# Kernel optimization log

Hardware: AMD Instinct MI355X
Metric: run time of the kernel (lower is better)

## Reference

```python
import jax, jax.numpy as jnp
import numpy as np

B, T, D, F, C = 16384, 256, 8, 512, 16  # batch, trees, depth, features, classes
L = 2 ** D  # leaves per tree


def setup_inputs() -> dict:
    key = jax.random.key(0)
    k1, k2, k3, k4 = jax.random.split(key, 4)
    x = jax.random.normal(k1, (B, F), dtype=jnp.float32)
    feature_weights = jax.random.normal(k2, (T, D, F), dtype=jnp.float32)
    thresholds = jax.random.normal(k3, (T, D), dtype=jnp.float32)
    responses = jax.random.normal(k4, (T, L, C), dtype=jnp.float32)
    return {"x": x, "feature_weights": feature_weights,
            "thresholds": thresholds, "responses": responses}


def reference(x, feature_weights, thresholds, responses):
    # Hard feature selection per (tree, level): argmax over features.
    fidx = jnp.argmax(feature_weights, axis=-1)            # [T, D] int
    fv = x[:, fidx]                                        # [B, T, D] gather
    bits = (fv > thresholds[None, :, :]).astype(x.dtype)   # [B, T, D]
    # decision = sum_d bit_d * 2^(D-1-d)  (matches decision*2+bit loop)
    powers = (2 ** jnp.arange(D - 1, -1, -1)).astype(x.dtype)  # [D]
    decision = jnp.sum(bits * powers, axis=-1).astype(jnp.int32)  # [B, T]
    # Gather leaf responses per (sample, tree) and average over trees.
    tree_ids = jnp.arange(T)[None, :]                      # [1, T]
    leaf_out = responses[tree_ids, decision]               # [B, T, C]
    out = jnp.mean(leaf_out, axis=1)                       # [B, C]
    return out  # dropout is identity at eval time
```

## Files before the change

kernel.cpp:

```cpp
#include <hip/hip_runtime.h>

constexpr int B = 16384;
constexpr int T = 256;
constexpr int D = 8;
constexpr int F = 512;
constexpr int C = 16;
constexpr int L = 256;

struct FP { int fidx; float thr; };

__global__ __launch_bounds__(256) void node_prep_kernel(
    const float* __restrict__ fw,
    const float* __restrict__ thr,
    FP* __restrict__ packed)
{
    const int wave = threadIdx.x >> 6;
    const int lane = threadIdx.x & 63;
    const int row  = blockIdx.x * 4 + wave;
    const float* base = fw + (size_t)row * F;

    float best = -INFINITY;
    int bidx = 0;
#pragma unroll
    for (int k = 0; k < F / 64; ++k) {
        const int idx = lane + k * 64;
        const float v = base[idx];
        if (v > best) { best = v; bidx = idx; }
    }
#pragma unroll
    for (int off = 32; off >= 1; off >>= 1) {
        const float ov = __shfl_xor(best, off);
        const int   oi = __shfl_xor(bidx, off);
        if (ov > best || (ov == best && oi < bidx)) { best = ov; bidx = oi; }
    }
    if (lane == 0) {
        FP p;
        p.fidx = bidx;
        p.thr  = thr[row];
        packed[row] = p;
    }
}

__global__ __launch_bounds__(256) void forest_kernel(
    const float* __restrict__ x,
    const FP* __restrict__ packed,
    const float* __restrict__ responses,
    float* __restrict__ out)
{
    __shared__ float xrow[4][F];
    __shared__ unsigned char sdec[4][T];

    const int b0  = blockIdx.x * 4;
    const int tid = threadIdx.x;

    {
        const float4* xs = reinterpret_cast<const float4*>(x + (size_t)b0 * F);
        float4* xl = reinterpret_cast<float4*>(&xrow[0][0]);
        xl[tid]       = xs[tid];
        xl[tid + 256] = xs[tid + 256];
    }
    __syncthreads();

    {
        const int2* p2 = reinterpret_cast<const int2*>(packed) + tid * D;
        int2 raw[D];
#pragma unroll
        for (int d = 0; d < D; ++d) raw[d] = p2[d];
        int dec0 = 0, dec1 = 0, dec2 = 0, dec3 = 0;
#pragma unroll
        for (int d = 0; d < D; ++d) {
            const int   f  = raw[d].x;
            const float th = __int_as_float(raw[d].y);
            const int   p  = 128 >> d;
            dec0 |= (xrow[0][f] > th) ? p : 0;
            dec1 |= (xrow[1][f] > th) ? p : 0;
            dec2 |= (xrow[2][f] > th) ? p : 0;
            dec3 |= (xrow[3][f] > th) ? p : 0;
        }
        sdec[0][tid] = (unsigned char)dec0;
        sdec[1][tid] = (unsigned char)dec1;
        sdec[2][tid] = (unsigned char)dec2;
        sdec[3][tid] = (unsigned char)dec3;
    }
    __syncthreads();

    const int w    = tid >> 6;
    const int lane = tid & 63;
    const int slot = lane >> 4;
    const int c    = lane & 15;
    const int sh   = slot * 8;

    float accA = 0.0f, accB = 0.0f;
    const int4* pdec = reinterpret_cast<const int4*>(&sdec[w][0]);

#define GATH(ACC, WD, TB)                                                  \
    {                                                                      \
        const int dd = ((WD) >> sh) & 255;                                 \
        const int t  = (TB) + slot;                                        \
        ACC += responses[((size_t)(((t) << 8) | dd) << 4) + c];            \
    }

#pragma unroll
    for (int kk = 0; kk < 16; ++kk) {
        const int4 pd = pdec[kk];
        GATH(accA, pd.x, kk * 16 + 0)
        GATH(accB, pd.y, kk * 16 + 4)
        GATH(accA, pd.z, kk * 16 + 8)
        GATH(accB, pd.w, kk * 16 + 12)
    }
#undef GATH

    float acc = accA + accB;
    acc += __shfl_xor(acc, 16);
    acc += __shfl_xor(acc, 32);

    if (lane < 16) out[(size_t)(b0 + w) * C + lane] = acc * (1.0f / T);
}

extern "C" void kernel_launch(void* const* d_in, const int* in_sizes, int n_in,
                              void* d_out, int out_size, void* d_ws, size_t ws_size,
                              hipStream_t stream) {
    const float* x         = (const float*)d_in[0];
    const float* fw        = (const float*)d_in[1];
    const float* thr       = (const float*)d_in[2];
    const float* responses = (const float*)d_in[3];
    float* out             = (float*)d_out;

    FP* packed = (FP*)d_ws;

    node_prep_kernel<<<(T * D) / 4, 256, 0, stream>>>(fw, thr, packed);
    forest_kernel<<<B / 4, 256, 0, stream>>>(x, packed, responses, out);
}
```

Measured before the change: 125.4 us.

## Gather leaf responses as float4 per lane with 16-tree strided mapping

Rewrites the response-gather phase so each lane loads a float4 (four classes) instead of a scalar. A lane now covers 16 trees spaced 16 apart, using a new lane-to-tree mapping and byte selection from the shared decision words. All 16 loads are issued up front, then the four partial class groups are combined with a wider shuffle reduction and written with a float4 store. It also adds a min-blocks hint to launch bounds. The aim is fewer load instructions and more memory-level parallelism, at the cost of extra registers for the 16 float4 buffers.

```diff
diff --git a/kernel.cpp b/kernel.cpp
--- a/kernel.cpp
+++ b/kernel.cpp
@@ -41,7 +41,7 @@
     }
 }
 
-__global__ __launch_bounds__(256) void forest_kernel(
+__global__ __launch_bounds__(256, 4) void forest_kernel(
     const float* __restrict__ x,
     const FP* __restrict__ packed,
     const float* __restrict__ responses,
@@ -86,35 +86,44 @@
 
     const int w    = tid >> 6;
     const int lane = tid & 63;
-    const int slot = lane >> 4;
-    const int c    = lane & 15;
-    const int sh   = slot * 8;
 
-    float accA = 0.0f, accB = 0.0f;
-    const int4* pdec = reinterpret_cast<const int4*>(&sdec[w][0]);
+    const int* pw   = reinterpret_cast<const int*>(&sdec[w][0]);
+    const int wsel  = lane >> 4;
+    const int bsel  = ((lane >> 2) & 3) * 8;
+    int dw[16];
+#pragma unroll
+    for (int kk = 0; kk < 16; ++kk) dw[kk] = pw[4 * kk + wsel];
 
-#define GATH(ACC, WD, TB)                                                  \
-    {                                                                      \
-        const int dd = ((WD) >> sh) & 255;                                 \
-        const int t  = (TB) + slot;                                        \
-        ACC += responses[((size_t)(((t) << 8) | dd) << 4) + c];            \
+    const int lbase = ((lane >> 2) << 12) | ((lane & 3) << 2);
+
+    float4 r[16];
+#pragma unroll
+    for (int kk = 0; kk < 16; ++kk) {
+        const int dd = (dw[kk] >> bsel) & 255;
+        r[kk] = *reinterpret_cast<const float4*>(
+            responses + (kk << 16) + (dd << 4) + lbase);
+    }
+
+    float4 acc = r[0];
+#pragma unroll
+    for (int kk = 1; kk < 16; ++kk) {
+        acc.x += r[kk].x; acc.y += r[kk].y;
+        acc.z += r[kk].z; acc.w += r[kk].w;
     }
 
 #pragma unroll
-    for (int kk = 0; kk < 16; ++kk) {
-        const int4 pd = pdec[kk];
-        GATH(accA, pd.x, kk * 16 + 0)
-        GATH(accB, pd.y, kk * 16 + 4)
-        GATH(accA, pd.z, kk * 16 + 8)
-        GATH(accB, pd.w, kk * 16 + 12)
+    for (int off = 4; off <= 32; off <<= 1) {
+        acc.x += __shfl_xor(acc.x, off);
+        acc.y += __shfl_xor(acc.y, off);
+        acc.z += __shfl_xor(acc.z, off);
+        acc.w += __shfl_xor(acc.w, off);
     }
-#undef GATH
 
-    float acc = accA + accB;
-    acc += __shfl_xor(acc, 16);
-    acc += __shfl_xor(acc, 32);
-
-    if (lane < 16) out[(size_t)(b0 + w) * C + lane] = acc * (1.0f / T);
+    if (lane < 4) {
+        const float s = 1.0f / T;
+        float4 o = make_float4(acc.x * s, acc.y * s, acc.z * s, acc.w * s);
+        *reinterpret_cast<float4*>(out + ((size_t)(b0 + w) << 4) + (lane << 2)) = o;
+    }
 }
 
 extern "C" void kernel_launch(void* const* d_in, const int* in_sizes, int n_in,
```

Result: faster. 103.2 us (-17.7%).
